# Kernel optimization log

Hardware: AMD Instinct MI355X
Metric: run time of the kernel (lower is better)

The kernel has to match this reference:

```python
import jax, jax.numpy as jnp
import numpy as np

BS, CIN, H, W = 1, 128, 448, 96
CLASSES = (8, 8, 8)
PAD = (0, 4, 4)
DIV = 1  # c3_line_div
K2 = H * CLASSES[0]                 # 3584 CondMul experts for stage 2
K3 = H * CLASSES[0] * CLASSES[1]    # 28672 CondMul experts for stage 3
C1_DIMS = [(128, 32), (32, 32), (32, 8)]
C2_DIMS = [(128, 32), (32, 32), (32, 16)]
C3_DIMS = [(128, 32), (32, 32), (32, 16)]


def _cond_mul(x, inds, w, b):
    # per-row expert gather then small matmul: [N,i] x [N,i,o] -> [N,o]
    return jnp.einsum('ni,nio->no', x, w[inds]) + b[inds]


def setup_inputs() -> dict:
    key = jax.random.key(0)
    ks = jax.random.split(key, 19)
    d = {'x_in': jax.random.normal(ks[0], (BS, CIN, H, W), jnp.float32)}
    k = 1
    for tag, dims, nexp in (('1', C1_DIMS, H), ('2', C2_DIMS, K2), ('3', C3_DIMS, K3)):
        for i, (ci, co) in enumerate(dims):
            if tag == '1':
                d['w1_%d' % i] = jax.random.normal(ks[k], (H, co, ci), jnp.float32) * 0.1
            else:
                d['w%s_%d' % (tag, i)] = jax.random.normal(ks[k], (nexp, ci, co), jnp.float32) * 0.1
            d['b%s_%d' % (tag, i)] = jax.random.normal(ks[k + 1], (nexp, co), jnp.float32) * 0.1
            k += 2
    return d


def reference(x_in, w1_0, b1_0, w1_1, b1_1, w1_2, b1_2,
              w2_0, b2_0, w2_1, b2_1, w2_2, b2_2,
              w3_0, b3_0, w3_1, b3_1, w3_2, b3_2):
    bs, cin, h, w = x_in.shape
    c12 = CLASSES[0] * CLASSES[1]
    c123 = c12 * CLASSES[2]
    lrelu = jax.nn.leaky_relu  # slope 0.01, matches F.leaky_relu default
    hoff = jnp.arange(h, dtype=jnp.int32)[None, :, None]  # [1,H,1] line offsets

    # stage 1: grouped 1x1 conv (one group per image line)
    x = jnp.transpose(x_in, (0, 2, 1, 3))  # [bs,H,C,W]
    x = lrelu(jnp.einsum('hoi,bhiw->bhow', w1_0, x) + b1_0[None, :, :, None])
    x = lrelu(jnp.einsum('hoi,bhiw->bhow', w1_1, x) + b1_1[None, :, :, None])
    x = jnp.einsum('hoi,bhiw->bhow', w1_2, x) + b1_2[None, :, :, None]  # [bs,H,cls1,W]
    inds1 = jnp.argmax(x, axis=2).astype(jnp.int32)  # [bs,H,W]
    inds1_l = (inds1 + CLASSES[0] * hoff).reshape(-1)  # [N]

    x_l = jnp.transpose(x_in, (0, 2, 3, 1)).reshape(-1, cin)  # [N,C], N=bs*H*W

    # stage 2: CondMul cascade routed by inds1
    x = lrelu(_cond_mul(x_l, inds1_l, w2_0, b2_0))
    x = lrelu(_cond_mul(x, inds1_l, w2_1, b2_1))
    x = _cond_mul(x, inds1_l, w2_2, b2_2)
    inds2 = jnp.argmax(x, axis=-1).astype(jnp.int32).reshape(bs, h, w)
    inds12 = inds1 * CLASSES[1] + (inds2 - PAD[1])
    inds12_cl = jnp.clip(inds12, 0, c12 - 1)
    inds12_l = (inds12_cl + c12 * hoff).reshape(-1)
    inds12_s = (inds12_cl + c12 * (hoff // DIV)).reshape(-1)

    # stage 3: CondMul cascade routed by inds12
    x = lrelu(_cond_mul(x_l, inds12_s, w3_0, b3_0))
    x = lrelu(_cond_mul(x, inds12_s, w3_1, b3_1))
    x3 = _cond_mul(x, inds12_l, w3_2, b3_2)  # [N, cls3+2*pad3]
    inds3 = jnp.argmax(x3, axis=-1).astype(jnp.int32).reshape(bs, h, w)

    inds123 = jnp.clip(inds12 * CLASSES[2] + (inds3 - PAD[2]), 0, c123 - 1)
    return inds123.reshape(bs, 1, h, w)
```

## Files before the change

kernel.cpp:

```cpp
#include <hip/hip_runtime.h>

#define H_ 448
#define W_ 96
#define CIN_ 128
#define HW_ (H_*W_)

__device__ __forceinline__ float lrelu(float v){ return v > 0.0f ? v : 0.01f*v; }

template<int NC>
__device__ __forceinline__ void sort_by_class(const unsigned char* s_cls, short* s_perm,
                                              int* s_cnt, int* s_off, int t)
{
    if (t < NC){
        int c = 0;
        for (int p = 0; p < 96; p++) if (s_cls[p] == (unsigned char)t) c++;
        s_cnt[t] = c;
    }
    __syncthreads();
    if (t == 0){
        int a = 0;
        for (int c = 0; c < NC; c++){ s_off[c] = a; a += s_cnt[c]; }
    }
    __syncthreads();
    if (t < NC){
        int o = s_off[t];
        for (int p = 0; p < 96; p++) if (s_cls[p] == (unsigned char)t) s_perm[o++] = (short)p;
    }
    __syncthreads();
}

__global__ __launch_bounds__(384, 3)
void cls3_fused(const float* __restrict__ X,
                const float* __restrict__ w1_0, const float* __restrict__ b1_0,
                const float* __restrict__ w1_1, const float* __restrict__ b1_1,
                const float* __restrict__ w1_2, const float* __restrict__ b1_2,
                const float* __restrict__ w2_0, const float* __restrict__ b2_0,
                const float* __restrict__ w2_1, const float* __restrict__ b2_1,
                const float* __restrict__ w2_2, const float* __restrict__ b2_2,
                const float* __restrict__ w3_0, const float* __restrict__ b3_0,
                const float* __restrict__ w3_1, const float* __restrict__ b3_1,
                const float* __restrict__ w3_2, const float* __restrict__ b3_2,
                int* __restrict__ out)
{
    __shared__ float s_w0[4096];
    __shared__ float s_w1[1024];
    __shared__ float s_w2[256];
    __shared__ float s_A[96*36];
    __shared__ float s_B[96*36];
    __shared__ unsigned char s_cls[96];
    __shared__ short s_perm[96];
    __shared__ int   s_raw[96];
    __shared__ int   s_cnt[64];
    __shared__ int   s_off[64];

    const int h  = blockIdx.x;
    const int t  = threadIdx.x;

    {
        const int w  = t % 96;
        const int s  = t / 96;
        const int hw = h*96 + w;

        const float* g0 = w1_0 + (size_t)h*4096;
        for (int j = t; j < 4096; j += 384) s_w0[j] = g0[j];
        const float* g1 = w1_1 + (size_t)h*1024;
        for (int j = t; j < 1024; j += 384) s_w1[j] = g1[j];
        const float* g2 = w1_2 + (size_t)h*256;
        for (int j = t; j < 256; j += 384) s_w2[j] = g2[j];
        __syncthreads();

        {
            float acc[8];
            const float* bp = b1_0 + h*32 + s*8;
            #pragma unroll
            for (int k=0;k<8;k++) acc[k] = bp[k];
            #pragma unroll 4
            for (int i4=0;i4<32;i4++){
                const float x0 = X[(size_t)(4*i4+0)*HW_ + hw];
                const float x1 = X[(size_t)(4*i4+1)*HW_ + hw];
                const float x2 = X[(size_t)(4*i4+2)*HW_ + hw];
                const float x3 = X[(size_t)(4*i4+3)*HW_ + hw];
                #pragma unroll
                for (int k=0;k<8;k++){
                    const float4 q = *(const float4*)&s_w0[(s*8+k)*128 + 4*i4];
                    acc[k] += x0*q.x; acc[k] += x1*q.y; acc[k] += x2*q.z; acc[k] += x3*q.w;
                }
            }
            #pragma unroll
            for (int k=0;k<8;k++) s_A[w*33 + s*8 + k] = lrelu(acc[k]);
        }
        __syncthreads();

        {
            float acc[8];
            const float* bp = b1_1 + h*32 + s*8;
            #pragma unroll
            for (int k=0;k<8;k++) acc[k] = bp[k];
            #pragma unroll
            for (int i4=0;i4<8;i4++){
                const float x0 = s_A[w*33 + 4*i4+0];
                const float x1 = s_A[w*33 + 4*i4+1];
                const float x2 = s_A[w*33 + 4*i4+2];
                const float x3 = s_A[w*33 + 4*i4+3];
                #pragma unroll
                for (int k=0;k<8;k++){
                    const float4 q = *(const float4*)&s_w1[(s*8+k)*32 + 4*i4];
                    acc[k] += x0*q.x; acc[k] += x1*q.y; acc[k] += x2*q.z; acc[k] += x3*q.w;
                }
            }
            #pragma unroll
            for (int k=0;k<8;k++) s_B[w*33 + s*8 + k] = lrelu(acc[k]);
        }
        __syncthreads();

        {
            float acc[2];
            const float* bp = b1_2 + h*8 + s*2;
            acc[0] = bp[0]; acc[1] = bp[1];
            #pragma unroll
            for (int i4=0;i4<8;i4++){
                const float x0 = s_B[w*33 + 4*i4+0];
                const float x1 = s_B[w*33 + 4*i4+1];
                const float x2 = s_B[w*33 + 4*i4+2];
                const float x3 = s_B[w*33 + 4*i4+3];
                #pragma unroll
                for (int k=0;k<2;k++){
                    const float4 q = *(const float4*)&s_w2[(s*2+k)*32 + 4*i4];
                    acc[k] += x0*q.x; acc[k] += x1*q.y; acc[k] += x2*q.z; acc[k] += x3*q.w;
                }
            }
            s_A[w*33 + s*2 + 0] = acc[0];
            s_A[w*33 + s*2 + 1] = acc[1];
        }
        __syncthreads();

        if (s == 0){
            const float* sc = &s_A[w*33];
            float best = sc[0]; int bi = 0;
            #pragma unroll
            for (int k=1;k<8;k++){ const float v = sc[k]; if (v > best){ best = v; bi = k; } }
            s_cls[w] = (unsigned char)bi;
        }
        __syncthreads();
    }

    sort_by_class<8>(s_cls, s_perm, s_cnt, s_off, t);

    const int p = t >> 2;
    const int q = t & 3;
    {
        const int sp = s_perm[p];
        const int c  = s_cls[sp];
        const long e = (long)h*8 + c;
        const int hw = h*96 + sp;
        const float* W0 = w2_0 + e*4096 + q*8;
        const float* W1 = w2_1 + e*1024 + q*8;
        const float* W2 = w2_2 + e*512  + q*4;

        float acc[8];
        {
            const float4 bv0 = *(const float4*)&b2_0[e*32 + q*8];
            const float4 bv1 = *(const float4*)&b2_0[e*32 + q*8 + 4];
            acc[0]=bv0.x; acc[1]=bv0.y; acc[2]=bv0.z; acc[3]=bv0.w;
            acc[4]=bv1.x; acc[5]=bv1.y; acc[6]=bv1.z; acc[7]=bv1.w;
        }
        #pragma unroll 8
        for (int i=0;i<128;i++){
            const float xv = X[(size_t)i*HW_ + hw];
            const float4 a = *(const float4*)&W0[i*32];
            const float4 b = *(const float4*)&W0[i*32 + 4];
            acc[0]+=xv*a.x; acc[1]+=xv*a.y; acc[2]+=xv*a.z; acc[3]+=xv*a.w;
            acc[4]+=xv*b.x; acc[5]+=xv*b.y; acc[6]+=xv*b.z; acc[7]+=xv*b.w;
        }
        *(float4*)&s_A[p*36 + q*8]     = make_float4(lrelu(acc[0]),lrelu(acc[1]),lrelu(acc[2]),lrelu(acc[3]));
        *(float4*)&s_A[p*36 + q*8 + 4] = make_float4(lrelu(acc[4]),lrelu(acc[5]),lrelu(acc[6]),lrelu(acc[7]));
        __syncthreads();

        float ac2[8];
        {
            const float4 bv0 = *(const float4*)&b2_1[e*32 + q*8];
            const float4 bv1 = *(const float4*)&b2_1[e*32 + q*8 + 4];
            ac2[0]=bv0.x; ac2[1]=bv0.y; ac2[2]=bv0.z; ac2[3]=bv0.w;
            ac2[4]=bv1.x; ac2[5]=bv1.y; ac2[6]=bv1.z; ac2[7]=bv1.w;
        }
        #pragma unroll 8
        for (int i=0;i<32;i++){
            const float xv = s_A[p*36 + i];
            const float4 a = *(const float4*)&W1[i*32];
            const float4 b = *(const float4*)&W1[i*32 + 4];
            ac2[0]+=xv*a.x; ac2[1]+=xv*a.y; ac2[2]+=xv*a.z; ac2[3]+=xv*a.w;
            ac2[4]+=xv*b.x; ac2[5]+=xv*b.y; ac2[6]+=xv*b.z; ac2[7]+=xv*b.w;
        }
        *(float4*)&s_B[p*36 + q*8]     = make_float4(lrelu(ac2[0]),lrelu(ac2[1]),lrelu(ac2[2]),lrelu(ac2[3]));
        *(float4*)&s_B[p*36 + q*8 + 4] = make_float4(lrelu(ac2[4]),lrelu(ac2[5]),lrelu(ac2[6]),lrelu(ac2[7]));
        __syncthreads();

        float4 sc = *(const float4*)&b2_2[e*16 + q*4];
        #pragma unroll 8
        for (int i=0;i<32;i++){
            const float xv = s_B[p*36 + i];
            const float4 r = *(const float4*)&W2[i*16];
            sc.x += xv*r.x; sc.y += xv*r.y; sc.z += xv*r.z; sc.w += xv*r.w;
        }
        float best = sc.x; int bi = q*4;
        if (sc.y > best){ best = sc.y; bi = q*4+1; }
        if (sc.z > best){ best = sc.z; bi = q*4+2; }
        if (sc.w > best){ best = sc.w; bi = q*4+3; }
        #pragma unroll
        for (int off=1; off<4; off<<=1){
            const float ob = __shfl_xor(best, off, 64);
            const int  obi = __shfl_xor(bi,  off, 64);
            if (ob > best || (ob == best && obi < bi)){ best = ob; bi = obi; }
        }
        __syncthreads();
        if (q == 0){
            const int raw = c*8 + bi - 4;
            s_raw[sp] = raw;
            s_cls[sp] = (unsigned char)(raw < 0 ? 0 : (raw > 63 ? 63 : raw));
        }
        __syncthreads();
    }

    sort_by_class<64>(s_cls, s_perm, s_cnt, s_off, t);

    {
        const int sp = s_perm[p];
        const int c  = s_cls[sp];
        const long e = (long)h*64 + c;
        const int hw = h*96 + sp;
        const float* W0 = w3_0 + e*4096 + q*8;
        const float* W1 = w3_1 + e*1024 + q*8;
        const float* W2 = w3_2 + e*512  + q*4;

        float acc[8];
        {
            const float4 bv0 = *(const float4*)&b3_0[e*32 + q*8];
            const float4 bv1 = *(const float4*)&b3_0[e*32 + q*8 + 4];
            acc[0]=bv0.x; acc[1]=bv0.y; acc[2]=bv0.z; acc[3]=bv0.w;
            acc[4]=bv1.x; acc[5]=bv1.y; acc[6]=bv1.z; acc[7]=bv1.w;
        }
        #pragma unroll 8
        for (int i=0;i<128;i++){
            const float xv = X[(size_t)i*HW_ + hw];
            const float4 a = *(const float4*)&W0[i*32];
            const float4 b = *(const float4*)&W0[i*32 + 4];
            acc[0]+=xv*a.x; acc[1]+=xv*a.y; acc[2]+=xv*a.z; acc[3]+=xv*a.w;
            acc[4]+=xv*b.x; acc[5]+=xv*b.y; acc[6]+=xv*b.z; acc[7]+=xv*b.w;
        }
        *(float4*)&s_A[p*36 + q*8]     = make_float4(lrelu(acc[0]),lrelu(acc[1]),lrelu(acc[2]),lrelu(acc[3]));
        *(float4*)&s_A[p*36 + q*8 + 4] = make_float4(lrelu(acc[4]),lrelu(acc[5]),lrelu(acc[6]),lrelu(acc[7]));
        __syncthreads();

        float ac2[8];
        {
            const float4 bv0 = *(const float4*)&b3_1[e*32 + q*8];
            const float4 bv1 = *(const float4*)&b3_1[e*32 + q*8 + 4];
            ac2[0]=bv0.x; ac2[1]=bv0.y; ac2[2]=bv0.z; ac2[3]=bv0.w;
            ac2[4]=bv1.x; ac2[5]=bv1.y; ac2[6]=bv1.z; ac2[7]=bv1.w;
        }
        #pragma unroll 8
        for (int i=0;i<32;i++){
            const float xv = s_A[p*36 + i];
            const float4 a = *(const float4*)&W1[i*32];
            const float4 b = *(const float4*)&W1[i*32 + 4];
            ac2[0]+=xv*a.x; ac2[1]+=xv*a.y; ac2[2]+=xv*a.z; ac2[3]+=xv*a.w;
            ac2[4]+=xv*b.x; ac2[5]+=xv*b.y; ac2[6]+=xv*b.z; ac2[7]+=xv*b.w;
        }
        *(float4*)&s_B[p*36 + q*8]     = make_float4(lrelu(ac2[0]),lrelu(ac2[1]),lrelu(ac2[2]),lrelu(ac2[3]));
        *(float4*)&s_B[p*36 + q*8 + 4] = make_float4(lrelu(ac2[4]),lrelu(ac2[5]),lrelu(ac2[6]),lrelu(ac2[7]));
        __syncthreads();

        float4 sc = *(const float4*)&b3_2[e*16 + q*4];
        #pragma unroll 8
        for (int i=0;i<32;i++){
            const float xv = s_B[p*36 + i];
            const float4 r = *(const float4*)&W2[i*16];
            sc.x += xv*r.x; sc.y += xv*r.y; sc.z += xv*r.z; sc.w += xv*r.w;
        }
        float best = sc.x; int bi = q*4;
        if (sc.y > best){ best = sc.y; bi = q*4+1; }
        if (sc.z > best){ best = sc.z; bi = q*4+2; }
        if (sc.w > best){ best = sc.w; bi = q*4+3; }
        #pragma unroll
        for (int off=1; off<4; off<<=1){
            const float ob = __shfl_xor(best, off, 64);
            const int  obi = __shfl_xor(bi,  off, 64);
            if (ob > best || (ob == best && obi < bi)){ best = ob; bi = obi; }
        }
        if (q == 0){
            int v = s_raw[sp]*8 + bi - 4;
            v = v < 0 ? 0 : (v > 511 ? 511 : v);
            out[h*96 + sp] = v;
        }
    }
}

extern "C" void kernel_launch(void* const* d_in, const int* in_sizes, int n_in,
                              void* d_out, int out_size, void* d_ws, size_t ws_size,
                              hipStream_t stream) {
    const float* X    = (const float*)d_in[0];
    const float* w1_0 = (const float*)d_in[1];
    const float* b1_0 = (const float*)d_in[2];
    const float* w1_1 = (const float*)d_in[3];
    const float* b1_1 = (const float*)d_in[4];
    const float* w1_2 = (const float*)d_in[5];
    const float* b1_2 = (const float*)d_in[6];
    const float* w2_0 = (const float*)d_in[7];
    const float* b2_0 = (const float*)d_in[8];
    const float* w2_1 = (const float*)d_in[9];
    const float* b2_1 = (const float*)d_in[10];
    const float* w2_2 = (const float*)d_in[11];
    const float* b2_2 = (const float*)d_in[12];
    const float* w3_0 = (const float*)d_in[13];
    const float* b3_0 = (const float*)d_in[14];
    const float* w3_1 = (const float*)d_in[15];
    const float* b3_1 = (const float*)d_in[16];
    const float* w3_2 = (const float*)d_in[17];
    const float* b3_2 = (const float*)d_in[18];
    int* out = (int*)d_out;

    cls3_fused<<<H_, 384, 0, stream>>>(X,
        w1_0, b1_0, w1_1, b1_1, w1_2, b1_2,
        w2_0, b2_0, w2_1, b2_1, w2_2, b2_2,
        w3_0, b3_0, w3_1, b3_1, w3_2, b3_2,
        out);
}
```

Before: 169.3 us.

## Split each image line across two blocks and narrow per-thread output width

```diff
diff --git a/kernel.cpp b/kernel.cpp
--- a/kernel.cpp
+++ b/kernel.cpp
@@ -4,6 +4,7 @@
 #define W_ 96
 #define CIN_ 128
 #define HW_ (H_*W_)
+#define PPB 48
 
 __device__ __forceinline__ float lrelu(float v){ return v > 0.0f ? v : 0.01f*v; }
 
@@ -13,7 +14,7 @@
 {
     if (t < NC){
         int c = 0;
-        for (int p = 0; p < 96; p++) if (s_cls[p] == (unsigned char)t) c++;
+        for (int p = 0; p < PPB; p++) if (s_cls[p] == (unsigned char)t) c++;
         s_cnt[t] = c;
     }
     __syncthreads();
@@ -24,12 +25,12 @@
     __syncthreads();
     if (t < NC){
         int o = s_off[t];
-        for (int p = 0; p < 96; p++) if (s_cls[p] == (unsigned char)t) s_perm[o++] = (short)p;
+        for (int p = 0; p < PPB; p++) if (s_cls[p] == (unsigned char)t) s_perm[o++] = (short)p;
     }
     __syncthreads();
 }
 
-__global__ __launch_bounds__(384, 3)
+__global__ __launch_bounds__(384, 6)
 void cls3_fused(const float* __restrict__ X,
                 const float* __restrict__ w1_0, const float* __restrict__ b1_0,
                 const float* __restrict__ w1_1, const float* __restrict__ b1_1,
@@ -45,21 +46,22 @@
     __shared__ float s_w0[4096];
     __shared__ float s_w1[1024];
     __shared__ float s_w2[256];
-    __shared__ float s_A[96*36];
-    __shared__ float s_B[96*36];
-    __shared__ unsigned char s_cls[96];
-    __shared__ short s_perm[96];
-    __shared__ int   s_raw[96];
+    __shared__ float s_A[PPB*36];
+    __shared__ float s_B[PPB*36];
+    __shared__ unsigned char s_cls[PPB];
+    __shared__ short s_perm[PPB];
+    __shared__ int   s_raw[PPB];
     __shared__ int   s_cnt[64];
     __shared__ int   s_off[64];
 
-    const int h  = blockIdx.x;
+    const int h  = blockIdx.x >> 1;
+    const int wb = (blockIdx.x & 1) * PPB;
     const int t  = threadIdx.x;
 
     {
-        const int w  = t % 96;
-        const int s  = t / 96;
-        const int hw = h*96 + w;
+        const int w  = t % PPB;
+        const int s  = t / PPB;
+        const int hw = h*96 + wb + w;
 
         const float* g0 = w1_0 + (size_t)h*4096;
         for (int j = t; j < 4096; j += 384) s_w0[j] = g0[j];
@@ -70,10 +72,10 @@
         __syncthreads();
 
         {
-            float acc[8];
-            const float* bp = b1_0 + h*32 + s*8;
-            #pragma unroll
-            for (int k=0;k<8;k++) acc[k] = bp[k];
+            float acc[4];
+            const float* bp = b1_0 + h*32 + s*4;
+            #pragma unroll
+            for (int k=0;k<4;k++) acc[k] = bp[k];
             #pragma unroll 4
             for (int i4=0;i4<32;i4++){
                 const float x0 = X[(size_t)(4*i4+0)*HW_ + hw];
@@ -81,21 +83,21 @@
                 const float x2 = X[(size_t)(4*i4+2)*HW_ + hw];
                 const float x3 = X[(size_t)(4*i4+3)*HW_ + hw];
                 #pragma unroll
-                for (int k=0;k<8;k++){
-                    const float4 q = *(const float4*)&s_w0[(s*8+k)*128 + 4*i4];
+                for (int k=0;k<4;k++){
+                    const float4 q = *(const float4*)&s_w0[(s*4+k)*128 + 4*i4];
                     acc[k] += x0*q.x; acc[k] += x1*q.y; acc[k] += x2*q.z; acc[k] += x3*q.w;
                 }
             }
             #pragma unroll
-            for (int k=0;k<8;k++) s_A[w*33 + s*8 + k] = lrelu(acc[k]);
+            for (int k=0;k<4;k++) s_A[w*33 + s*4 + k] = lrelu(acc[k]);
         }
         __syncthreads();
 
         {
-            float acc[8];
-            const float* bp = b1_1 + h*32 + s*8;
-            #pragma unroll
-            for (int k=0;k<8;k++) acc[k] = bp[k];
+            float acc[4];
+            const float* bp = b1_1 + h*32 + s*4;
+            #pragma unroll
+            for (int k=0;k<4;k++) acc[k] = bp[k];
             #pragma unroll
             for (int i4=0;i4<8;i4++){
                 const float x0 = s_A[w*33 + 4*i4+0];
@@ -103,34 +105,27 @@
                 const float x2 = s_A[w*33 + 4*i4+2];
                 const float x3 = s_A[w*33 + 4*i4+3];
                 #pragma unroll
-                for (int k=0;k<8;k++){
-                    const float4 q = *(const float4*)&s_w1[(s*8+k)*32 + 4*i4];
+                for (int k=0;k<4;k++){
+                    const float4 q = *(const float4*)&s_w1[(s*4+k)*32 + 4*i4];
                     acc[k] += x0*q.x; acc[k] += x1*q.y; acc[k] += x2*q.z; acc[k] += x3*q.w;
                 }
             }
             #pragma unroll
-            for (int k=0;k<8;k++) s_B[w*33 + s*8 + k] = lrelu(acc[k]);
+            for (int k=0;k<4;k++) s_B[w*33 + s*4 + k] = lrelu(acc[k]);
         }
         __syncthreads();
 
         {
-            float acc[2];
-            const float* bp = b1_2 + h*8 + s*2;
-            acc[0] = bp[0]; acc[1] = bp[1];
+            float acc = b1_2[h*8 + s];
             #pragma unroll
             for (int i4=0;i4<8;i4++){
-                const float x0 = s_B[w*33 + 4*i4+0];
-                const float x1 = s_B[w*33 + 4*i4+1];
-                const float x2 = s_B[w*33 + 4*i4+2];
-                const float x3 = s_B[w*33 + 4*i4+3];
-                #pragma unroll
-                for (int k=0;k<2;k++){
-                    const float4 q = *(const float4*)&s_w2[(s*2+k)*32 + 4*i4];
-                    acc[k] += x0*q.x; acc[k] += x1*q.y; acc[k] += x2*q.z; acc[k] += x3*q.w;
-                }
+                const float4 q = *(const float4*)&s_w2[s*32 + 4*i4];
+                acc += s_B[w*33 + 4*i4+0]*q.x;
+                acc += s_B[w*33 + 4*i4+1]*q.y;
+                acc += s_B[w*33 + 4*i4+2]*q.z;
+                acc += s_B[w*33 + 4*i4+3]*q.w;
             }
-            s_A[w*33 + s*2 + 0] = acc[0];
-            s_A[w*33 + s*2 + 1] = acc[1];
+            s_A[w*33 + s] = acc;
         }
         __syncthreads();
 
@@ -146,74 +141,54 @@
 
     sort_by_class<8>(s_cls, s_perm, s_cnt, s_off, t);
 
-    const int p = t >> 2;
-    const int q = t & 3;
+    const int p = t >> 3;
+    const int j = t & 7;
     {
         const int sp = s_perm[p];
         const int c  = s_cls[sp];
         const long e = (long)h*8 + c;
-        const int hw = h*96 + sp;
-        const float* W0 = w2_0 + e*4096 + q*8;
-        const float* W1 = w2_1 + e*1024 + q*8;
-        const float* W2 = w2_2 + e*512  + q*4;
-
-        float acc[8];
-        {
-            const float4 bv0 = *(const float4*)&b2_0[e*32 + q*8];
-            const float4 bv1 = *(const float4*)&b2_0[e*32 + q*8 + 4];
-            acc[0]=bv0.x; acc[1]=bv0.y; acc[2]=bv0.z; acc[3]=bv0.w;
-            acc[4]=bv1.x; acc[5]=bv1.y; acc[6]=bv1.z; acc[7]=bv1.w;
-        }
+        const int hw = h*96 + wb + sp;
+        const float* W0 = w2_0 + e*4096 + j*4;
+        const float* W1 = w2_1 + e*1024 + j*4;
+        const float* W2 = w2_2 + e*512  + j*2;
+
+        float4 acc = *(const float4*)&b2_0[e*32 + j*4];
         #pragma unroll 8
         for (int i=0;i<128;i++){
             const float xv = X[(size_t)i*HW_ + hw];
-            const float4 a = *(const float4*)&W0[i*32];
-            const float4 b = *(const float4*)&W0[i*32 + 4];
-            acc[0]+=xv*a.x; acc[1]+=xv*a.y; acc[2]+=xv*a.z; acc[3]+=xv*a.w;
-            acc[4]+=xv*b.x; acc[5]+=xv*b.y; acc[6]+=xv*b.z; acc[7]+=xv*b.w;
-        }
-        *(float4*)&s_A[p*36 + q*8]     = make_float4(lrelu(acc[0]),lrelu(acc[1]),lrelu(acc[2]),lrelu(acc[3]));
-        *(float4*)&s_A[p*36 + q*8 + 4] = make_float4(lrelu(acc[4]),lrelu(acc[5]),lrelu(acc[6]),lrelu(acc[7]));
-        __syncthreads();
-
-        float ac2[8];
-        {
-            const float4 bv0 = *(const float4*)&b2_1[e*32 + q*8];
-            const float4 bv1 = *(const float4*)&b2_1[e*32 + q*8 + 4];
-            ac2[0]=bv0.x; ac2[1]=bv0.y; ac2[2]=bv0.z; ac2[3]=bv0.w;
-            ac2[4]=bv1.x; ac2[5]=bv1.y; ac2[6]=bv1.z; ac2[7]=bv1.w;
-        }
+            const float4 q = *(const float4*)&W0[i*32];
+            acc.x += xv*q.x; acc.y += xv*q.y; acc.z += xv*q.z; acc.w += xv*q.w;
+        }
+        *(float4*)&s_A[p*36 + j*4] = make_float4(lrelu(acc.x),lrelu(acc.y),lrelu(acc.z),lrelu(acc.w));
+        __syncthreads();
+
+        float4 ac2 = *(const float4*)&b2_1[e*32 + j*4];
         #pragma unroll 8
         for (int i=0;i<32;i++){
             const float xv = s_A[p*36 + i];
-            const float4 a = *(const float4*)&W1[i*32];
-            const float4 b = *(const float4*)&W1[i*32 + 4];
-            ac2[0]+=xv*a.x; ac2[1]+=xv*a.y; ac2[2]+=xv*a.z; ac2[3]+=xv*a.w;
-            ac2[4]+=xv*b.x; ac2[5]+=xv*b.y; ac2[6]+=xv*b.z; ac2[7]+=xv*b.w;
-        }
-        *(float4*)&s_B[p*36 + q*8]     = make_float4(lrelu(ac2[0]),lrelu(ac2[1]),lrelu(ac2[2]),lrelu(ac2[3]));
-        *(float4*)&s_B[p*36 + q*8 + 4] = make_float4(lrelu(ac2[4]),lrelu(ac2[5]),lrelu(ac2[6]),lrelu(ac2[7]));
-        __syncthreads();
-
-        float4 sc = *(const float4*)&b2_2[e*16 + q*4];
+            const float4 q = *(const float4*)&W1[i*32];
+            ac2.x += xv*q.x; ac2.y += xv*q.y; ac2.z += xv*q.z; ac2.w += xv*q.w;
+        }
+        *(float4*)&s_B[p*36 + j*4] = make_float4(lrelu(ac2.x),lrelu(ac2.y),lrelu(ac2.z),lrelu(ac2.w));
+        __syncthreads();
+
+        float2 sc = *(const float2*)&b2_2[e*16 + j*2];
         #pragma unroll 8
         for (int i=0;i<32;i++){
             const float xv = s_B[p*36 + i];
-            const float4 r = *(const float4*)&W2[i*16];
-            sc.x += xv*r.x; sc.y += xv*r.y; sc.z += xv*r.z; sc.w += xv*r.w;
-        }
-        float best = sc.x; int bi = q*4;
-        if (sc.y > best){ best = sc.y; bi = q*4+1; }
-        if (sc.z > best){ best = sc.z; bi = q*4+2; }
-        if (sc.w > best){ best = sc.w; bi = q*4+3; }
+            const float2 r = *(const float2*)&W2[i*16];
+            sc.x += xv*r.x; sc.y += xv*r.y;
+        }
+        float best = sc.x; int bi = j*2;
+        if (sc.y > best){ best = sc.y; bi = j*2+1; }
         #pragma unroll
-        for (int off=1; off<4; off<<=1){
+        for (int off=1; off<8; off<<=1){
             const float ob = __shfl_xor(best, off, 64);
             const int  obi = __shfl_xor(bi,  off, 64);
             if (ob > best || (ob == best && obi < bi)){ best = ob; bi = obi; }
         }
         __syncthreads();
-        if (q == 0){
+        if (j == 0){
             const int raw = c*8 + bi - 4;
             s_raw[sp] = raw;
             s_cls[sp] = (unsigned char)(raw < 0 ? 0 : (raw > 63 ? 63 : raw));
@@ -227,70 +202,50 @@
         const int sp = s_perm[p];
         const int c  = s_cls[sp];
         const long e = (long)h*64 + c;
-        const int hw = h*96 + sp;
-        const float* W0 = w3_0 + e*4096 + q*8;
-        const float* W1 = w3_1 + e*1024 + q*8;
-        const float* W2 = w3_2 + e*512  + q*4;
-
-        float acc[8];
-        {
-            const float4 bv0 = *(const float4*)&b3_0[e*32 + q*8];
-            const float4 bv1 = *(const float4*)&b3_0[e*32 + q*8 + 4];
-            acc[0]=bv0.x; acc[1]=bv0.y; acc[2]=bv0.z; acc[3]=bv0.w;
-            acc[4]=bv1.x; acc[5]=bv1.y; acc[6]=bv1.z; acc[7]=bv1.w;
-        }
+        const int hw = h*96 + wb + sp;
+        const float* W0 = w3_0 + e*4096 + j*4;
+        const float* W1 = w3_1 + e*1024 + j*4;
+        const float* W2 = w3_2 + e*512  + j*2;
+
+        float4 acc = *(const float4*)&b3_0[e*32 + j*4];
         #pragma unroll 8
         for (int i=0;i<128;i++){
             const float xv = X[(size_t)i*HW_ + hw];
-            const float4 a = *(const float4*)&W0[i*32];
-            const float4 b = *(const float4*)&W0[i*32 + 4];
-            acc[0]+=xv*a.x; acc[1]+=xv*a.y; acc[2]+=xv*a.z; acc[3]+=xv*a.w;
-            acc[4]+=xv*b.x; acc[5]+=xv*b.y; acc[6]+=xv*b.z; acc[7]+=xv*b.w;
-        }
-        *(float4*)&s_A[p*36 + q*8]     = make_float4(lrelu(acc[0]),lrelu(acc[1]),lrelu(acc[2]),lrelu(acc[3]));
-        *(float4*)&s_A[p*36 + q*8 + 4] = make_float4(lrelu(acc[4]),lrelu(acc[5]),lrelu(acc[6]),lrelu(acc[7]));
-        __syncthreads();
-
-        float ac2[8];
-        {
-            const float4 bv0 = *(const float4*)&b3_1[e*32 + q*8];
-            const float4 bv1 = *(const float4*)&b3_1[e*32 + q*8 + 4];
-            ac2[0]=bv0.x; ac2[1]=bv0.y; ac2[2]=bv0.z; ac2[3]=bv0.w;
-            ac2[4]=bv1.x; ac2[5]=bv1.y; ac2[6]=bv1.z; ac2[7]=bv1.w;
-        }
+            const float4 q = *(const float4*)&W0[i*32];
+            acc.x += xv*q.x; acc.y += xv*q.y; acc.z += xv*q.z; acc.w += xv*q.w;
+        }
+        *(float4*)&s_A[p*36 + j*4] = make_float4(lrelu(acc.x),lrelu(acc.y),lrelu(acc.z),lrelu(acc.w));
+        __syncthreads();
+
+        float4 ac2 = *(const float4*)&b3_1[e*32 + j*4];
         #pragma unroll 8
         for (int i=0;i<32;i++){
             const float xv = s_A[p*36 + i];
-            const float4 a = *(const float4*)&W1[i*32];
-            const float4 b = *(const float4*)&W1[i*32 + 4];
-            ac2[0]+=xv*a.x; ac2[1]+=xv*a.y; ac2[2]+=xv*a.z; ac2[3]+=xv*a.w;
-            ac2[4]+=xv*b.x; ac2[5]+=xv*b.y; ac2[6]+=xv*b.z; ac2[7]+=xv*b.w;
-        }
-        *(float4*)&s_B[p*36 + q*8]     = make_float4(lrelu(ac2[0]),lrelu(ac2[1]),lrelu(ac2[2]),lrelu(ac2[3]));
-        *(float4*)&s_B[p*36 + q*8 + 4] = make_float4(lrelu(ac2[4]),lrelu(ac2[5]),lrelu(ac2[6]),lrelu(ac2[7]));
-        __syncthreads();
-
-        float4 sc = *(const float4*)&b3_2[e*16 + q*4];
+            const float4 q = *(const float4*)&W1[i*32];
+            ac2.x += xv*q.x; ac2.y += xv*q.y; ac2.z += xv*q.z; ac2.w += xv*q.w;
+        }
+        *(float4*)&s_B[p*36 + j*4] = make_float4(lrelu(ac2.x),lrelu(ac2.y),lrelu(ac2.z),lrelu(ac2.w));
+        __syncthreads();
+
+        float2 sc = *(const float2*)&b3_2[e*16 + j*2];
         #pragma unroll 8
         for (int i=0;i<32;i++){
             const float xv = s_B[p*36 + i];
-            const float4 r = *(const float4*)&W2[i*16];
-            sc.x += xv*r.x; sc.y += xv*r.y; sc.z += xv*r.z; sc.w += xv*r.w;
-        }
-        float best = sc.x; int bi = q*4;
-        if (sc.y > best){ best = sc.y; bi = q*4+1; }
-        if (sc.z > best){ best = sc.z; bi = q*4+2; }
-        if (sc.w > best){ best = sc.w; bi = q*4+3; }
+            const float2 r = *(const float2*)&W2[i*16];
+            sc.x += xv*r.x; sc.y += xv*r.y;
+        }
+        float best = sc.x; int bi = j*2;
+        if (sc.y > best){ best = sc.y; bi = j*2+1; }
         #pragma unroll
-        for (int off=1; off<4; off<<=1){
+        for (int off=1; off<8; off<<=1){
             const float ob = __shfl_xor(best, off, 64);
             const int  obi = __shfl_xor(bi,  off, 64);
             if (ob > best || (ob == best && obi < bi)){ best = ob; bi = obi; }
         }
-        if (q == 0){
+        if (j == 0){
             int v = s_raw[sp]*8 + bi - 4;
             v = v < 0 ? 0 : (v > 511 ? 511 : v);
-            out[h*96 + sp] = v;
+            out[h*96 + wb + sp] = v;
         }
     }
 }
@@ -319,7 +274,7 @@
     const float* b3_2 = (const float*)d_in[18];
     int* out = (int*)d_out;
 
-    cls3_fused<<<H_, 384, 0, stream>>>(X,
+    cls3_fused<<<H_*2, 384, 0, stream>>>(X,
         w1_0, b1_0, w1_1, b1_1, w1_2, b1_2,
         w2_0, b2_0, w2_1, b2_1, w2_2, b2_2,
         w3_0, b3_0, w3_1, b3_1, w3_2, b3_2,
```

Measured after the change: 152.5 us. -9.9%, faster.
